# Optimization experiments

Hardware: AMD Instinct MI355X
Metric: run time of the kernel (lower is better)

Reference implementation:

```python
import jax, jax.numpy as jnp
import numpy as np

B, S, D, H = 4, 2048, 1024, 16
DK = D // H


def setup_inputs() -> dict:
    key = jax.random.key(0)
    ks = jax.random.split(key, 11)
    scale = 1.0 / np.sqrt(D)
    inp = {
        "query": jax.random.normal(ks[0], (B, S, D), jnp.float32),
        "key": jax.random.normal(ks[1], (B, S, D), jnp.float32),
        "value": jax.random.normal(ks[2], (B, S, D), jnp.float32),
    }
    # 4 linear layers: Wq, Wk, Wv, Wo (torch Linear: y = x @ W.T + b)
    for i, name in enumerate(["q", "k", "v", "o"]):
        inp[f"W{name}"] = jax.random.uniform(ks[3 + 2 * i], (D, D), jnp.float32, -scale, scale)
        inp[f"b{name}"] = jax.random.uniform(ks[4 + 2 * i], (D,), jnp.float32, -scale, scale)
    return inp


def reference(query, key, value, Wq, bq, Wk, bk, Wv, bv, Wo, bo):
    def proj(x, W, b):
        # [B,S,D] -> [B,H,S,DK]
        y = x @ W.T + b
        return y.reshape(B, S, H, DK).transpose(0, 2, 1, 3)

    q = proj(query, Wq, bq)
    k = proj(key, Wk, bk)
    v = proj(value, Wv, bv)
    scores = jnp.einsum("bhqd,bhkd->bhqk", q, k) / jnp.sqrt(jnp.float32(DK))
    p = jax.nn.softmax(scores, axis=-1)  # dropout p=0 -> identity
    ctx = jnp.einsum("bhqk,bhkd->bhqd", p, v)
    ctx = ctx.transpose(0, 2, 1, 3).reshape(B, S, D)
    return ctx @ Wo.T + bo
```

## Files before the change

### kernel.cpp

```cpp
#include <hip/hip_runtime.h>

typedef unsigned short u16;
typedef unsigned int u32;
typedef __attribute__((ext_vector_type(8))) short short8v;
typedef __attribute__((ext_vector_type(4))) short short4v;
typedef __attribute__((ext_vector_type(4))) float floatx4;

#define BB 4
#define SS 2048
#define DD 1024
#define HH 16
#define DKK 64
#define MM (BB * SS)
#define KK DD
#define NN DD
#define QSCALE 0.18033688011112042f

#define PS_RS 12
#define PS_CS 200
#define PS_REGION 1600

__device__ __forceinline__ u16 f2bf(float f) {
  union { __bf16 h; u16 u; } r; r.h = (__bf16)f; return r.u;
}
__device__ __forceinline__ u32 pack2bf(float a, float b) {
  union { u32 u; __bf16 h[2]; } r;
  r.h[0] = (__bf16)a; r.h[1] = (__bf16)b; return r.u;
}
__device__ __forceinline__ short8v cat44(short4v a, short4v b) {
  return __builtin_shufflevector(a, b, 0, 1, 2, 3, 4, 5, 6, 7);
}

__device__ __forceinline__ void load_lds16(const void* g, void* l) {
  __builtin_amdgcn_global_load_lds((const __attribute__((address_space(1))) void*)g,
                                   (__attribute__((address_space(3))) void*)l, 16, 0, 0);
}

__device__ __forceinline__ floatx4 mfma_k32(short8v a, short8v b, floatx4 c) {
  return __builtin_amdgcn_mfma_f32_16x16x32_bf16(a, b, c, 0, 0, 0);
}

__global__ __launch_bounds__(256) void cvt_w4(const float* __restrict__ w0,
                                              const float* __restrict__ w1,
                                              const float* __restrict__ w2,
                                              const float* __restrict__ w3,
                                              u16* __restrict__ out) {
  const int y = blockIdx.y;
  const float* in = (y == 0) ? w0 : (y == 1) ? w1 : (y == 2) ? w2 : w3;
  u16* o = out + (size_t)y * DD * DD;
  const int i = (blockIdx.x * 256 + threadIdx.x) * 8;
  float4 a = *(const float4*)(in + i);
  float4 b = *(const float4*)(in + i + 4);
  uint4 v;
  v.x = pack2bf(a.x, a.y); v.y = pack2bf(a.z, a.w);
  v.z = pack2bf(b.x, b.y); v.w = pack2bf(b.z, b.w);
  *(uint4*)(o + i) = v;
}

__global__ __launch_bounds__(256) void cvt_a3(const float* __restrict__ a0,
                                              const float* __restrict__ a1,
                                              const float* __restrict__ a2,
                                              u16* __restrict__ o0, u16* __restrict__ o1,
                                              u16* __restrict__ o2) {
  const int y = blockIdx.y;
  const float* in = (y == 0) ? a0 : (y == 1) ? a1 : a2;
  u16* o = (y == 0) ? o0 : (y == 1) ? o1 : o2;
  const int i = (blockIdx.x * 256 + threadIdx.x) * 8;
  float4 a = *(const float4*)(in + i);
  float4 b = *(const float4*)(in + i + 4);
  uint4 v;
  v.x = pack2bf(a.x, a.y); v.y = pack2bf(a.z, a.w);
  v.z = pack2bf(b.x, b.y); v.w = pack2bf(b.z, b.w);
  *(uint4*)(o + i) = v;
}

__device__ __forceinline__ void gemm_tile(const u16* __restrict__ A, const u16* __restrict__ W,
                                          u16* As, u16* Bs, floatx4 (&acc)[4][4]) {
  const int tid = threadIdx.x;
  const int w = tid >> 6, lane = tid & 63;
  const int lr = lane & 15, lq = lane >> 4;
  const int wr = w >> 1, wc = w & 1;
  const u16* ga0 = A + (size_t)(2 * w * 16 + lr) * KK + lq * 8;
  const u16* ga1 = ga0 + 16 * KK;
  const u16* gb0 = W + (size_t)(2 * w * 16 + lr) * KK + lq * 8;
  const u16* gb1 = gb0 + 16 * KK;
  u16* la0 = &As[(2 * w) * 512]; u16* la1 = la0 + 512;
  u16* lb0 = &Bs[(2 * w) * 512]; u16* lb1 = lb0 + 512;

  load_lds16(ga0, la0); load_lds16(ga1, la1);
  load_lds16(gb0, lb0); load_lds16(gb1, lb1);

  for (int k0 = 0; k0 < KK; k0 += 32) {
    __syncthreads();
    short8v af[4], bf[4];
#pragma unroll
    for (int i = 0; i < 4; ++i) {
      af[i] = *(const short8v*)&As[(wr * 4 + i) * 512 + lane * 8];
      bf[i] = *(const short8v*)&Bs[(wc * 4 + i) * 512 + lane * 8];
    }
    __syncthreads();
    if (k0 + 32 < KK) {
      load_lds16(ga0 + k0 + 32, la0); load_lds16(ga1 + k0 + 32, la1);
      load_lds16(gb0 + k0 + 32, lb0); load_lds16(gb1 + k0 + 32, lb1);
    }
#pragma unroll
    for (int i = 0; i < 4; ++i)
#pragma unroll
      for (int j = 0; j < 4; ++j)
        acc[i][j] = mfma_k32(af[i], bf[j], acc[i][j]);
  }
}

__global__ __launch_bounds__(256) void proj_gemm(
    const u16* __restrict__ qc, const u16* __restrict__ kc, const u16* __restrict__ vc,
    const u16* __restrict__ Wq, const u16* __restrict__ Wk, const u16* __restrict__ Wv,
    const float* __restrict__ bq, const float* __restrict__ bk, const float* __restrict__ bv,
    u16* __restrict__ Qb, u16* __restrict__ Kb, u16* __restrict__ Vtb) {
  __shared__ __align__(16) u16 As[128 * 32];
  __shared__ __align__(16) u16 Bs[128 * 32];
  const int z = blockIdx.z;
  const u16* A = (z == 0) ? qc : (z == 1) ? kc : vc;
  const u16* W = (z == 0) ? Wq : (z == 1) ? Wk : Wv;
  const float* bias = (z == 0) ? bq : (z == 1) ? bk : bv;
  const int m0 = blockIdx.x * 128, n0 = blockIdx.y * 128;

  floatx4 acc[4][4] = {};
  gemm_tile(A + (size_t)m0 * KK, W + (size_t)n0 * KK, As, Bs, acc);

  const int tid = threadIdx.x;
  const int w = tid >> 6, lane = tid & 63;
  const int lr = lane & 15, lq = lane >> 4;
  const int wr = w >> 1, wc = w & 1;

  if (z == 2) {
#pragma unroll
    for (int j = 0; j < 4; ++j) {
      const int col = n0 + wc * 64 + j * 16 + lr;
      const float bv_ = bias[col];
      const int h = col >> 6, dk = col & 63;
#pragma unroll
      for (int i = 0; i < 4; ++i) {
        const int row = m0 + wr * 64 + i * 16 + lq * 4;
        const int b = row >> 11, s = row & (SS - 1);
        uint2 pk;
        pk.x = pack2bf(acc[i][j][0] + bv_, acc[i][j][1] + bv_);
        pk.y = pack2bf(acc[i][j][2] + bv_, acc[i][j][3] + bv_);
        *(uint2*)&Vtb[(((size_t)(b * HH + h)) * DKK + dk) * SS + s] = pk;
      }
    }
  } else {
    u16* out = (z == 0) ? Qb : Kb;
    const float sc = (z == 0) ? QSCALE : 1.0f;
#pragma unroll
    for (int j = 0; j < 4; ++j) {
      const int col = n0 + wc * 64 + j * 16 + lr;
      const float bv_ = bias[col];
#pragma unroll
      for (int i = 0; i < 4; ++i)
#pragma unroll
        for (int r = 0; r < 4; ++r) {
          const int row = m0 + wr * 64 + i * 16 + lq * 4 + r;
          out[(size_t)row * NN + col] = f2bf((acc[i][j][r] + bv_) * sc);
        }
    }
  }
}

__global__ __launch_bounds__(256) void out_gemm(const u16* __restrict__ A,
                                                const u16* __restrict__ W,
                                                const float* __restrict__ bias,
                                                float* __restrict__ out) {
  __shared__ __align__(16) u16 As[128 * 32];
  __shared__ __align__(16) u16 Bs[128 * 32];
  const int m0 = blockIdx.x * 128, n0 = blockIdx.y * 128;
  floatx4 acc[4][4] = {};
  gemm_tile(A + (size_t)m0 * KK, W + (size_t)n0 * KK, As, Bs, acc);

  const int tid = threadIdx.x;
  const int w = tid >> 6, lane = tid & 63;
  const int lr = lane & 15, lq = lane >> 4;
  const int wr = w >> 1, wc = w & 1;
#pragma unroll
  for (int j = 0; j < 4; ++j) {
    const int col = n0 + wc * 64 + j * 16 + lr;
    const float bv = bias[col];
#pragma unroll
    for (int i = 0; i < 4; ++i)
#pragma unroll
      for (int r = 0; r < 4; ++r) {
        const int row = m0 + wr * 64 + i * 16 + lq * 4 + r;
        out[(size_t)row * NN + col] = acc[i][j][r] + bv;
      }
  }
}

__global__ __launch_bounds__(256, 4) void attn_kernel(const u16* __restrict__ Q,
                                                      const u16* __restrict__ Kmat,
                                                      const u16* __restrict__ Vt,
                                                      u16* __restrict__ ctx) {
  __shared__ __align__(16) u16 Ks[64 * 64];
  __shared__ __align__(16) u16 Vs[64 * 64];
  __shared__ __align__(16) u16 Ps[4 * PS_REGION];
  const int tid = threadIdx.x;
  const int w = tid >> 6, lane = tid & 63;
  const int lr = lane & 15, lq = lane >> 4;
  const int bh = blockIdx.x, b = bh >> 4, h = bh & 15;
  const int q0 = blockIdx.y * 128;

  short8v qf[2][2];
  {
    const u16* qp = Q + ((size_t)(b * SS + q0 + w * 32 + lr)) * DD + h * 64 + lq * 8;
    qf[0][0] = *(const short8v*)qp;
    qf[0][1] = *(const short8v*)(qp + 32);
    qf[1][0] = *(const short8v*)(qp + 16 * DD);
    qf[1][1] = *(const short8v*)(qp + 16 * DD + 32);
  }
  floatx4 o[2][4] = {};
  float l_part[2][4] = {};

  const u16* kp = Kmat + ((size_t)(b * SS + w * 16 + lr)) * DD + h * 64 + lq * 8;
  const u16* vp = Vt + (((size_t)(b * HH + h)) * DKK + w * 16 + lr) * SS + lq * 8;

  for (int kt = 0; kt < SS / 64; ++kt) {
    load_lds16(kp,      &Ks[(2 * w) * 512]);
    load_lds16(kp + 32, &Ks[(2 * w + 1) * 512]);
    load_lds16(vp,      &Vs[(2 * w) * 512]);
    load_lds16(vp + 32, &Vs[(2 * w + 1) * 512]);
    kp += 64 * DD; vp += 64;
    __syncthreads();

    floatx4 sc[2][4] = {};
#pragma unroll
    for (int t = 0; t < 4; ++t) {
      short8v kb0 = *(const short8v*)&Ks[t * 1024 + lane * 8];
      short8v kb1 = *(const short8v*)&Ks[t * 1024 + 512 + lane * 8];
#pragma unroll
      for (int s = 0; s < 2; ++s) {
        sc[s][t] = mfma_k32(qf[s][0], kb0, sc[s][t]);
        sc[s][t] = mfma_k32(qf[s][1], kb1, sc[s][t]);
      }
    }

    short8v pa[2][2];
#pragma unroll
    for (int s = 0; s < 2; ++s) {
#pragma unroll
      for (int t = 0; t < 4; ++t) {
#pragma unroll
        for (int r = 0; r < 4; ++r) {
          const float e = __builtin_amdgcn_exp2f(sc[s][t][r]);
          sc[s][t][r] = e;
          l_part[s][r] += e;
        }
      }
      u16* pw = &Ps[w * PS_REGION];
#pragma unroll
      for (int t = 0; t < 4; ++t) {
        const int base = (2 * t + (lr >> 3)) * PS_CS + (lr & 7);
#pragma unroll
        for (int r = 0; r < 4; ++r)
          pw[base + (lq * 4 + r) * PS_RS] = f2bf(sc[s][t][r]);
      }
      {
        const u16* rp0 = pw + lq * PS_CS + lr * PS_RS;
        const u16* rp1 = pw + (4 + lq) * PS_CS + lr * PS_RS;
        pa[s][0] = cat44(*(const short4v*)rp0, *(const short4v*)(rp0 + 4));
        pa[s][1] = cat44(*(const short4v*)rp1, *(const short4v*)(rp1 + 4));
      }
    }

#pragma unroll
    for (int t = 0; t < 4; ++t) {
      short8v vb0 = *(const short8v*)&Vs[t * 1024 + lane * 8];
      short8v vb1 = *(const short8v*)&Vs[t * 1024 + 512 + lane * 8];
#pragma unroll
      for (int s = 0; s < 2; ++s) {
        o[s][t] = mfma_k32(pa[s][0], vb0, o[s][t]);
        o[s][t] = mfma_k32(pa[s][1], vb1, o[s][t]);
      }
    }
    __syncthreads();
  }

  float inv[2][4];
#pragma unroll
  for (int s = 0; s < 2; ++s)
#pragma unroll
    for (int r = 0; r < 4; ++r) {
      float l = l_part[s][r];
      l += __shfl_xor(l, 1); l += __shfl_xor(l, 2);
      l += __shfl_xor(l, 4); l += __shfl_xor(l, 8);
      inv[s][r] = 1.0f / l;
    }

#pragma unroll
  for (int s = 0; s < 2; ++s)
#pragma unroll
    for (int r = 0; r < 4; ++r) {
      const int sq = q0 + w * 32 + s * 16 + lq * 4 + r;
      u16* cp = ctx + ((size_t)(b * SS + sq)) * DD + h * 64;
      const float iv = inv[s][r];
#pragma unroll
      for (int t = 0; t < 4; ++t)
        cp[t * 16 + lr] = f2bf(o[s][t][r] * iv);
    }
}

extern "C" void kernel_launch(void* const* d_in, const int* in_sizes, int n_in,
                              void* d_out, int out_size, void* d_ws, size_t ws_size,
                              hipStream_t stream) {
  const float* query = (const float*)d_in[0];
  const float* key   = (const float*)d_in[1];
  const float* value = (const float*)d_in[2];
  const float* Wq = (const float*)d_in[3];  const float* bq = (const float*)d_in[4];
  const float* Wk = (const float*)d_in[5];  const float* bk = (const float*)d_in[6];
  const float* Wv = (const float*)d_in[7];  const float* bv = (const float*)d_in[8];
  const float* Wo = (const float*)d_in[9];  const float* bo = (const float*)d_in[10];
  float* out = (float*)d_out;

  char* ws = (char*)d_ws;
  size_t off = 0;
  u16* Wb   = (u16*)(ws + off); off += (size_t)4 * DD * DD * 2;
  u16* Qb   = (u16*)(ws + off); off += (size_t)MM * DD * 2;
  u16* Kb   = (u16*)(ws + off); off += (size_t)MM * DD * 2;
  u16* Vtb  = (u16*)(ws + off); off += (size_t)MM * DD * 2;
  u16* qc   = (u16*)(ws + off);
  u16* ctxb = qc;               off += (size_t)MM * DD * 2;
  u16* kc = (u16*)d_out;
  u16* vc = (u16*)d_out + (size_t)MM * DD;
  u16* Wq_b = Wb, *Wk_b = Wb + (size_t)DD * DD, *Wv_b = Wb + (size_t)2 * DD * DD,
     *Wo_b = Wb + (size_t)3 * DD * DD;

  const int wn = DD * DD, an = MM * DD;
  cvt_w4<<<dim3(wn / 2048, 4), 256, 0, stream>>>(Wq, Wk, Wv, Wo, Wb);
  cvt_a3<<<dim3(an / 2048, 3), 256, 0, stream>>>(query, key, value, qc, kc, vc);

  proj_gemm<<<dim3(MM / 128, NN / 128, 3), 256, 0, stream>>>(
      qc, kc, vc, Wq_b, Wk_b, Wv_b, bq, bk, bv, Qb, Kb, Vtb);

  attn_kernel<<<dim3(BB * HH, SS / 128), 256, 0, stream>>>(Qb, Kb, Vtb, ctxb);

  out_gemm<<<dim3(MM / 128, NN / 128), 256, 0, stream>>>(ctxb, Wo_b, bo, out);
}
```

Baseline: 389.1 us.

## Replace GEMM core with 256x256 tiled, swizzled, double-buffered 8-wave pipeline

Result: faster. 363.2 us (-6.7%).

```diff
diff --git a/kernel.cpp b/kernel.cpp
--- a/kernel.cpp
+++ b/kernel.cpp
@@ -74,77 +74,147 @@
   *(uint4*)(o + i) = v;
 }
 
-__device__ __forceinline__ void gemm_tile(const u16* __restrict__ A, const u16* __restrict__ W,
-                                          u16* As, u16* Bs, floatx4 (&acc)[4][4]) {
+#define NT (KK / 64)
+#define ITERS (NT / 2)
+
+__device__ __forceinline__ void stage_half(const u16* __restrict__ gsrc, u16* ldst,
+                                           int tid) {
+#pragma unroll
+  for (int L = 0; L < 2; ++L) {
+    const int s = L * 512 + tid;
+    const int r = s >> 3;
+    const int g = (s & 7) ^ (r & 7);
+    load_lds16(gsrc + (size_t)r * KK + g * 8, ldst + s * 8);
+  }
+}
+
+__device__ __forceinline__ void gemm256_core(const u16* __restrict__ A,
+                                             const u16* __restrict__ W,
+                                             u16* As, u16* Bs,
+                                             floatx4 (&acc)[8][4]) {
   const int tid = threadIdx.x;
   const int w = tid >> 6, lane = tid & 63;
-  const int lr = lane & 15, lq = lane >> 4;
-  const int wr = w >> 1, wc = w & 1;
-  const u16* ga0 = A + (size_t)(2 * w * 16 + lr) * KK + lq * 8;
-  const u16* ga1 = ga0 + 16 * KK;
-  const u16* gb0 = W + (size_t)(2 * w * 16 + lr) * KK + lq * 8;
-  const u16* gb1 = gb0 + 16 * KK;
-  u16* la0 = &As[(2 * w) * 512]; u16* la1 = la0 + 512;
-  u16* lb0 = &Bs[(2 * w) * 512]; u16* lb1 = lb0 + 512;
-
-  load_lds16(ga0, la0); load_lds16(ga1, la1);
-  load_lds16(gb0, lb0); load_lds16(gb1, lb1);
-
-  for (int k0 = 0; k0 < KK; k0 += 32) {
-    __syncthreads();
-    short8v af[4], bf[4];
-#pragma unroll
-    for (int i = 0; i < 4; ++i) {
-      af[i] = *(const short8v*)&As[(wr * 4 + i) * 512 + lane * 8];
-      bf[i] = *(const short8v*)&Bs[(wc * 4 + i) * 512 + lane * 8];
-    }
-    __syncthreads();
-    if (k0 + 32 < KK) {
-      load_lds16(ga0 + k0 + 32, la0); load_lds16(ga1 + k0 + 32, la1);
-      load_lds16(gb0 + k0 + 32, lb0); load_lds16(gb1 + k0 + 32, lb1);
-    }
-#pragma unroll
-    for (int i = 0; i < 4; ++i)
-#pragma unroll
-      for (int j = 0; j < 4; ++j)
-        acc[i][j] = mfma_k32(af[i], bf[j], acc[i][j]);
-  }
-}
-
-__global__ __launch_bounds__(256) void proj_gemm(
+  const int wm = w >> 2, wn = w & 3;
+  const int wnh = wn >> 1, wno = wn & 1;
+  const int lr = lane & 15;
+  const int c0 = (((lane >> 2) & 1) << 5) | ((((lane >> 4) ^ lane) & 3) << 3);
+
+#define AP(d, fr, kk) \
+  (*(const short8v*)(As + ((d)*2 + wm) * 8192 + ((fr)*16 + lr) * 64 + (c0 ^ ((kk)*32))))
+#define BP(d, fc, kk) \
+  (*(const short8v*)(Bs + ((d)*2 + wnh) * 8192 + (wno * 64 + (fc)*16 + lr) * 64 + (c0 ^ ((kk)*32))))
+#define MFMA8(FROFF, B, FCOFF)                                                  \
+  _Pragma("unroll") for (int fr_ = 0; fr_ < 4; ++fr_)                           \
+  _Pragma("unroll") for (int fc_ = 0; fc_ < 2; ++fc_) {                         \
+    acc[(FROFF) + fr_][(FCOFF) + fc_] =                                         \
+        mfma_k32(a[fr_][0], B[fc_][0], acc[(FROFF) + fr_][(FCOFF) + fc_]);      \
+    acc[(FROFF) + fr_][(FCOFF) + fc_] =                                         \
+        mfma_k32(a[fr_][1], B[fc_][1], acc[(FROFF) + fr_][(FCOFF) + fc_]);      \
+  }
+#define BAR() __builtin_amdgcn_s_barrier()
+#define PRIO1() __builtin_amdgcn_s_setprio(1)
+#define PRIO0() __builtin_amdgcn_s_setprio(0)
+
+  short8v a[4][2], b01[2][2], b23[2][2];
+
+  stage_half(A, As + 0 * 8192, tid);
+  stage_half(A + (size_t)128 * KK, As + 1 * 8192, tid);
+  stage_half(W, Bs + 0 * 8192, tid);
+  stage_half(W + (size_t)128 * KK, Bs + 1 * 8192, tid);
+  stage_half(W + 64, Bs + 2 * 8192, tid);
+  stage_half(W + (size_t)128 * KK + 64, Bs + 3 * 8192, tid);
+  asm volatile("s_waitcnt vmcnt(4)" ::: "memory");
+  BAR();
+
+#pragma unroll 1
+  for (int j = 0; j < ITERS; ++j) {
+    const int e = 2 * j, o = e + 1;
+    const bool haveE2 = (j + 1 < ITERS);
+#pragma unroll
+    for (int fr = 0; fr < 4; ++fr) { a[fr][0] = AP(0, fr, 0); a[fr][1] = AP(0, fr, 1); }
+#pragma unroll
+    for (int fc = 0; fc < 2; ++fc) { b01[fc][0] = BP(0, fc, 0); b01[fc][1] = BP(0, fc, 1); }
+    stage_half(A + (size_t)o * 64, As + 2 * 8192, tid);
+    BAR(); PRIO1(); MFMA8(0, b01, 0); PRIO0(); BAR();
+#pragma unroll
+    for (int fc = 0; fc < 2; ++fc) { b23[fc][0] = BP(0, fc + 2, 0); b23[fc][1] = BP(0, fc + 2, 1); }
+    stage_half(A + (size_t)128 * KK + (size_t)o * 64, As + 3 * 8192, tid);
+    BAR(); PRIO1(); MFMA8(0, b23, 2); PRIO0(); BAR();
+#pragma unroll
+    for (int fr = 0; fr < 4; ++fr) { a[fr][0] = AP(0, fr + 4, 0); a[fr][1] = AP(0, fr + 4, 1); }
+    if (haveE2) stage_half(W + (size_t)(e + 2) * 64, Bs + 0 * 8192, tid);
+    BAR(); PRIO1(); MFMA8(4, b01, 0); PRIO0(); BAR();
+    if (haveE2) {
+      stage_half(W + (size_t)128 * KK + (size_t)(e + 2) * 64, Bs + 1 * 8192, tid);
+      asm volatile("s_waitcnt vmcnt(4)" ::: "memory");
+    } else {
+      asm volatile("s_waitcnt vmcnt(0)" ::: "memory");
+    }
+    BAR(); PRIO1(); MFMA8(4, b23, 2); PRIO0(); BAR();
+#pragma unroll
+    for (int fr = 0; fr < 4; ++fr) { a[fr][0] = AP(1, fr, 0); a[fr][1] = AP(1, fr, 1); }
+#pragma unroll
+    for (int fc = 0; fc < 2; ++fc) { b01[fc][0] = BP(1, fc, 0); b01[fc][1] = BP(1, fc, 1); }
+    if (haveE2) stage_half(A + (size_t)(e + 2) * 64, As + 0 * 8192, tid);
+    BAR(); PRIO1(); MFMA8(0, b01, 0); PRIO0(); BAR();
+#pragma unroll
+    for (int fc = 0; fc < 2; ++fc) { b23[fc][0] = BP(1, fc + 2, 0); b23[fc][1] = BP(1, fc + 2, 1); }
+    if (haveE2) stage_half(A + (size_t)128 * KK + (size_t)(e + 2) * 64, As + 1 * 8192, tid);
+    BAR(); PRIO1(); MFMA8(0, b23, 2); PRIO0(); BAR();
+#pragma unroll
+    for (int fr = 0; fr < 4; ++fr) { a[fr][0] = AP(1, fr + 4, 0); a[fr][1] = AP(1, fr + 4, 1); }
+    if (haveE2) stage_half(W + (size_t)(o + 2) * 64, Bs + 2 * 8192, tid);
+    BAR(); PRIO1(); MFMA8(4, b01, 0); PRIO0(); BAR();
+    if (haveE2) {
+      stage_half(W + (size_t)128 * KK + (size_t)(o + 2) * 64, Bs + 3 * 8192, tid);
+      asm volatile("s_waitcnt vmcnt(4)" ::: "memory");
+    }
+    BAR(); PRIO1(); MFMA8(4, b23, 2); PRIO0(); BAR();
+  }
+#undef AP
+#undef BP
+#undef MFMA8
+#undef BAR
+#undef PRIO1
+#undef PRIO0
+}
+
+__global__ __launch_bounds__(512, 2) void proj_gemm(
     const u16* __restrict__ qc, const u16* __restrict__ kc, const u16* __restrict__ vc,
     const u16* __restrict__ Wq, const u16* __restrict__ Wk, const u16* __restrict__ Wv,
     const float* __restrict__ bq, const float* __restrict__ bk, const float* __restrict__ bv,
     u16* __restrict__ Qb, u16* __restrict__ Kb, u16* __restrict__ Vtb) {
-  __shared__ __align__(16) u16 As[128 * 32];
-  __shared__ __align__(16) u16 Bs[128 * 32];
+  __shared__ __align__(16) u16 As[2 * 2 * 8192];
+  __shared__ __align__(16) u16 Bs[2 * 2 * 8192];
   const int z = blockIdx.z;
   const u16* A = (z == 0) ? qc : (z == 1) ? kc : vc;
   const u16* W = (z == 0) ? Wq : (z == 1) ? Wk : Wv;
   const float* bias = (z == 0) ? bq : (z == 1) ? bk : bv;
-  const int m0 = blockIdx.x * 128, n0 = blockIdx.y * 128;
-
-  floatx4 acc[4][4] = {};
-  gemm_tile(A + (size_t)m0 * KK, W + (size_t)n0 * KK, As, Bs, acc);
+  const int m0 = blockIdx.x * 256, n0 = blockIdx.y * 256;
+
+  floatx4 acc[8][4] = {};
+  gemm256_core(A + (size_t)m0 * KK, W + (size_t)n0 * KK, As, Bs, acc);
 
   const int tid = threadIdx.x;
   const int w = tid >> 6, lane = tid & 63;
   const int lr = lane & 15, lq = lane >> 4;
-  const int wr = w >> 1, wc = w & 1;
+  const int wm = w >> 2, wn = w & 3;
+  const int row0 = m0 + wm * 128;
+  const int col0 = n0 + wn * 64;
 
   if (z == 2) {
 #pragma unroll
-    for (int j = 0; j < 4; ++j) {
-      const int col = n0 + wc * 64 + j * 16 + lr;
+    for (int fc = 0; fc < 4; ++fc) {
+      const int col = col0 + fc * 16 + lr;
       const float bv_ = bias[col];
       const int h = col >> 6, dk = col & 63;
 #pragma unroll
-      for (int i = 0; i < 4; ++i) {
-        const int row = m0 + wr * 64 + i * 16 + lq * 4;
+      for (int fr = 0; fr < 8; ++fr) {
+        const int row = row0 + fr * 16 + lq * 4;
         const int b = row >> 11, s = row & (SS - 1);
         uint2 pk;
-        pk.x = pack2bf(acc[i][j][0] + bv_, acc[i][j][1] + bv_);
-        pk.y = pack2bf(acc[i][j][2] + bv_, acc[i][j][3] + bv_);
+        pk.x = pack2bf(acc[fr][fc][0] + bv_, acc[fr][fc][1] + bv_);
+        pk.y = pack2bf(acc[fr][fc][2] + bv_, acc[fr][fc][3] + bv_);
         *(uint2*)&Vtb[(((size_t)(b * HH + h)) * DKK + dk) * SS + s] = pk;
       }
     }
@@ -152,44 +222,46 @@
     u16* out = (z == 0) ? Qb : Kb;
     const float sc = (z == 0) ? QSCALE : 1.0f;
 #pragma unroll
-    for (int j = 0; j < 4; ++j) {
-      const int col = n0 + wc * 64 + j * 16 + lr;
+    for (int fc = 0; fc < 4; ++fc) {
+      const int col = col0 + fc * 16 + lr;
       const float bv_ = bias[col];
 #pragma unroll
-      for (int i = 0; i < 4; ++i)
-#pragma unroll
-        for (int r = 0; r < 4; ++r) {
-          const int row = m0 + wr * 64 + i * 16 + lq * 4 + r;
-          out[(size_t)row * NN + col] = f2bf((acc[i][j][r] + bv_) * sc);
+      for (int fr = 0; fr < 8; ++fr)
+#pragma unroll
+        for (int rr = 0; rr < 4; ++rr) {
+          const int row = row0 + fr * 16 + lq * 4 + rr;
+          out[(size_t)row * NN + col] = f2bf((acc[fr][fc][rr] + bv_) * sc);
         }
     }
   }
 }
 
-__global__ __launch_bounds__(256) void out_gemm(const u16* __restrict__ A,
-                                                const u16* __restrict__ W,
-                                                const float* __restrict__ bias,
-                                                float* __restrict__ out) {
-  __shared__ __align__(16) u16 As[128 * 32];
-  __shared__ __align__(16) u16 Bs[128 * 32];
-  const int m0 = blockIdx.x * 128, n0 = blockIdx.y * 128;
-  floatx4 acc[4][4] = {};
-  gemm_tile(A + (size_t)m0 * KK, W + (size_t)n0 * KK, As, Bs, acc);
+__global__ __launch_bounds__(512, 2) void out_gemm(const u16* __restrict__ A,
+                                                   const u16* __restrict__ W,
+                                                   const float* __restrict__ bias,
+                                                   float* __restrict__ out) {
+  __shared__ __align__(16) u16 As[2 * 2 * 8192];
+  __shared__ __align__(16) u16 Bs[2 * 2 * 8192];
+  const int m0 = blockIdx.x * 256, n0 = blockIdx.y * 256;
+  floatx4 acc[8][4] = {};
+  gemm256_core(A + (size_t)m0 * KK, W + (size_t)n0 * KK, As, Bs, acc);
 
   const int tid = threadIdx.x;
   const int w = tid >> 6, lane = tid & 63;
   const int lr = lane & 15, lq = lane >> 4;
-  const int wr = w >> 1, wc = w & 1;
-#pragma unroll
-  for (int j = 0; j < 4; ++j) {
-    const int col = n0 + wc * 64 + j * 16 + lr;
+  const int wm = w >> 2, wn = w & 3;
+  const int row0 = m0 + wm * 128;
+  const int col0 = n0 + wn * 64;
+#pragma unroll
+  for (int fc = 0; fc < 4; ++fc) {
+    const int col = col0 + fc * 16 + lr;
     const float bv = bias[col];
 #pragma unroll
-    for (int i = 0; i < 4; ++i)
-#pragma unroll
-      for (int r = 0; r < 4; ++r) {
-        const int row = m0 + wr * 64 + i * 16 + lq * 4 + r;
-        out[(size_t)row * NN + col] = acc[i][j][r] + bv;
+    for (int fr = 0; fr < 8; ++fr)
+#pragma unroll
+      for (int rr = 0; rr < 4; ++rr) {
+        const int row = row0 + fr * 16 + lq * 4 + rr;
+        out[(size_t)row * NN + col] = acc[fr][fc][rr] + bv;
       }
   }
 }
@@ -335,10 +407,10 @@
   cvt_w4<<<dim3(wn / 2048, 4), 256, 0, stream>>>(Wq, Wk, Wv, Wo, Wb);
   cvt_a3<<<dim3(an / 2048, 3), 256, 0, stream>>>(query, key, value, qc, kc, vc);
 
-  proj_gemm<<<dim3(MM / 128, NN / 128, 3), 256, 0, stream>>>(
+  proj_gemm<<<dim3(MM / 256, NN / 256, 3), 512, 0, stream>>>(
       qc, kc, vc, Wq_b, Wk_b, Wv_b, bq, bk, bv, Qb, Kb, Vtb);
 
   attn_kernel<<<dim3(BB * HH, SS / 128), 256, 0, stream>>>(Qb, Kb, Vtb, ctxb);
 
-  out_gemm<<<dim3(MM / 128, NN / 128), 256, 0, stream>>>(ctxb, Wo_b, bo, out);
-}
+  out_gemm<<<dim3(MM / 256, NN / 256), 512, 0, stream>>>(ctxb, Wo_b, bo, out);
+}
```
